# Kernel optimization log

Hardware: AMD Instinct MI355X
Metric: run time of the kernel (lower is better)

Reference implementation:

```python
import jax, jax.numpy as jnp
import numpy as np

N_NODES = 100000


def _gcn_conv(x, W, b, src, dst, num_nodes):
    """PyG GCNConv: h = x @ W; symmetric-normalized scatter-add over edges
    (self-loops already included in src/dst); out = aggregate + b."""
    h = x @ W  # [N, out]
    ones = jnp.ones(src.shape[0], dtype=x.dtype)
    deg = jax.ops.segment_sum(ones, dst, num_segments=num_nodes)  # in-degree incl self-loop
    dinv = jnp.where(deg > 0, jax.lax.rsqrt(deg), 0.0)
    norm = dinv[src] * dinv[dst]  # [E]
    msg = h[src] * norm[:, None]  # [E, out] -- dominant memory traffic
    out = jax.ops.segment_sum(msg, dst, num_segments=num_nodes)
    return out + b


def setup_inputs() -> dict:
    key = jax.random.key(0)
    k = jax.random.split(key, 4)
    in_c, hid, out_c = 128, 64, 32
    n_edges = 1600000
    x = jax.random.normal(k[0], (N_NODES, in_c), dtype=jnp.float32)
    edge_index = jax.random.randint(k[1], (2, n_edges), 0, N_NODES, dtype=jnp.int64)
    W1 = jax.random.normal(k[2], (in_c, hid), dtype=jnp.float32) * (1.0 / np.sqrt(in_c))
    b1 = jnp.zeros((hid,), dtype=jnp.float32)
    W2 = jax.random.normal(k[3], (hid, out_c), dtype=jnp.float32) * (1.0 / np.sqrt(hid))
    b2 = jnp.zeros((out_c,), dtype=jnp.float32)
    return {"x": x, "edge_index": edge_index, "W1": W1, "b1": b1, "W2": W2, "b2": b2}


def reference(x, edge_index, W1, b1, W2, b2):
    num_nodes = x.shape[0]
    loops = jnp.arange(num_nodes, dtype=edge_index.dtype)
    src = jnp.concatenate([edge_index[0], loops])  # add self-loops once, shared by both layers
    dst = jnp.concatenate([edge_index[1], loops])
    h = _gcn_conv(x, W1, b1, src, dst, num_nodes)
    h = jax.nn.relu(h)
    out = _gcn_conv(h, W2, b2, src, dst, num_nodes)
    return out
```

## Files before the change

### kernel.cpp

```cpp
#include <hip/hip_runtime.h>


#define NBKT(n) (((n) + 127) >> 7)

__device__ inline float bf2f(unsigned short u) {
    union { unsigned int i; float f; } v;
    v.i = ((unsigned int)u) << 16;
    return v.f;
}
__device__ inline unsigned short f2bf(float f) {
    union { float f; unsigned int i; } v;
    v.f = f;
    unsigned int u = v.i;
    return (unsigned short)((u + 0x7fff + ((u >> 16) & 1)) >> 16);
}

#define BH_CHUNK 4096
__global__ void __launch_bounds__(256) bhist_kernel(
        const int* __restrict__ dst, int E, int nbk, int* __restrict__ bcnt) {
    __shared__ int cnt[NBKT(100000)];
    const int t = threadIdx.x;
    const int beg = blockIdx.x * BH_CHUNK;
    const int end = min(E, beg + BH_CHUNK);
    for (int b = t; b < nbk; b += 256) cnt[b] = 0;
    __syncthreads();
    for (int i = beg + t; i < end; i += 256) atomicAdd(&cnt[dst[i] >> 7], 1);
    __syncthreads();
    for (int b = t; b < nbk; b += 256) {
        int c = cnt[b];
        if (c) atomicAdd(&bcnt[b], c);
    }
}

__global__ void bscan_kernel(const int* __restrict__ bcnt, int nbk, int E,
                             int* __restrict__ boffs, int* __restrict__ gcursor) {
    __shared__ int s[1024];
    const int t = threadIdx.x;
    int v = (t < nbk) ? bcnt[t] : 0;
    s[t] = v;
    __syncthreads();
    for (int off = 1; off < 1024; off <<= 1) {
        int x = (t >= off) ? s[t - off] : 0;
        __syncthreads();
        s[t] += x;
        __syncthreads();
    }
    if (t < nbk) {
        int excl = s[t] - v;
        boffs[t] = excl;
        gcursor[t] = excl;
    }
    if (t == 0) boffs[nbk] = E;
}

#define BF_CHUNK 4096
__global__ void __launch_bounds__(256) binfill_kernel(
        const int* __restrict__ src, const int* __restrict__ dst, int E, int nbk,
        int* __restrict__ gcursor, int* __restrict__ entries) {
    __shared__ int cnt[NBKT(100000)];
    __shared__ int gbase[NBKT(100000)];
    __shared__ int rank[NBKT(100000)];
    const int t = threadIdx.x;
    const int beg = blockIdx.x * BF_CHUNK;
    const int end = min(E, beg + BF_CHUNK);
    for (int b = t; b < nbk; b += 256) cnt[b] = 0;
    __syncthreads();
    for (int i = beg + t; i < end; i += 256) atomicAdd(&cnt[dst[i] >> 7], 1);
    __syncthreads();
    for (int b = t; b < nbk; b += 256) {
        int c = cnt[b];
        gbase[b] = c ? atomicAdd(&gcursor[b], c) : 0;
        rank[b] = 0;
    }
    __syncthreads();
    for (int i = beg + t; i < end; i += 256) {
        int d = dst[i];
        int b = d >> 7;
        int r = atomicAdd(&rank[b], 1);
        entries[gbase[b] + r] = (src[i] << 7) | (d & 127);
    }
}

__global__ void __launch_bounds__(256) bucket2csr_kernel(
        const int* __restrict__ entries, const int* __restrict__ boffs, int nbk,
        int* __restrict__ offs, int* __restrict__ csr_src, float* __restrict__ dinv,
        int N, int E) {
    __shared__ int cnt[128];
    __shared__ int s[128];
    __shared__ int rank[128];
    const int t = threadIdx.x;
    const int b = blockIdx.x;
    const int beg = boffs[b];
    const int end = boffs[b + 1];
    if (t < 128) { cnt[t] = 0; rank[t] = 0; }
    __syncthreads();
    for (int i = beg + t; i < end; i += 256) atomicAdd(&cnt[entries[i] & 127], 1);
    __syncthreads();
    if (t < 128) s[t] = cnt[t];
    __syncthreads();
    for (int off = 1; off < 128; off <<= 1) {
        int x = 0;
        if (t < 128 && t >= off) x = s[t - off];
        __syncthreads();
        if (t < 128) s[t] += x;
        __syncthreads();
    }
    const int node0 = b * 128;
    if (t < 128 && node0 + t < N) {
        offs[node0 + t] = beg + s[t] - cnt[t];
        dinv[node0 + t] = rsqrtf((float)cnt[t] + 1.0f);
    }
    if (b == 0 && t == 0) offs[N] = E;
    __syncthreads();
    for (int i = beg + t; i < end; i += 256) {
        int e = entries[i];
        int d = e & 127;
        int r = atomicAdd(&rank[d], 1);
        csr_src[beg + s[d] - cnt[d] + r] = (int)((unsigned)e >> 7);
    }
}

#define FMA4(ACC, AV, WV) \
    ACC.x += (AV) * (WV).x; ACC.y += (AV) * (WV).y; ACC.z += (AV) * (WV).z; ACC.w += (AV) * (WV).w;

template <int K, int C, int BR, bool BF16OUT, bool BF16IN>
__global__ void __launch_bounds__(256) gemm_tile_kernel(
        const void* __restrict__ Av, const float* __restrict__ W,
        const float* __restrict__ dinv, void* __restrict__ outv, int N) {
    constexpr int F4R = K / 4;
    constexpr int CG = C / 4;
    static_assert(256 / CG * 4 == BR, "geometry");
    __shared__ float Wl[K * C];
    __shared__ float Al[BR * K];

    const int t = threadIdx.x;
    for (int i = t; i < K * C / 4; i += 256) ((float4*)Wl)[i] = ((const float4*)W)[i];
    const int row0 = blockIdx.x * BR;
    for (int i = t; i < BR * F4R; i += 256) {
        int r = i / F4R, k4 = i % F4R;
        float4 v = make_float4(0.f, 0.f, 0.f, 0.f);
        if (row0 + r < N) {
            if (BF16IN) {
                ushort4 u = ((const ushort4*)Av)[(size_t)(row0 + r) * F4R + k4];
                v.x = bf2f(u.x); v.y = bf2f(u.y); v.z = bf2f(u.z); v.w = bf2f(u.w);
            } else {
                v = ((const float4*)Av)[(size_t)(row0 + r) * F4R + k4];
            }
        }
        *(float4*)(Al + r * K + k4 * 4) = v;
    }
    __syncthreads();

    const int c0 = (t % CG) * 4;
    const int r0 = (t / CG) * 4;
    const float* Ab = Al + r0 * K;

    float4 acc0 = {0, 0, 0, 0}, acc1 = {0, 0, 0, 0}, acc2 = {0, 0, 0, 0}, acc3 = {0, 0, 0, 0};

#pragma unroll 2
    for (int k4 = 0; k4 < K / 4; ++k4) {
        float4 a0 = *(const float4*)(Ab + 0 * K + k4 * 4);
        float4 a1 = *(const float4*)(Ab + 1 * K + k4 * 4);
        float4 a2 = *(const float4*)(Ab + 2 * K + k4 * 4);
        float4 a3 = *(const float4*)(Ab + 3 * K + k4 * 4);
        float4 w0 = *(const float4*)(Wl + (k4 * 4 + 0) * C + c0);
        float4 w1 = *(const float4*)(Wl + (k4 * 4 + 1) * C + c0);
        float4 w2 = *(const float4*)(Wl + (k4 * 4 + 2) * C + c0);
        float4 w3 = *(const float4*)(Wl + (k4 * 4 + 3) * C + c0);
        FMA4(acc0, a0.x, w0) FMA4(acc1, a1.x, w0) FMA4(acc2, a2.x, w0) FMA4(acc3, a3.x, w0)
        FMA4(acc0, a0.y, w1) FMA4(acc1, a1.y, w1) FMA4(acc2, a2.y, w1) FMA4(acc3, a3.y, w1)
        FMA4(acc0, a0.z, w2) FMA4(acc1, a1.z, w2) FMA4(acc2, a2.z, w2) FMA4(acc3, a3.z, w2)
        FMA4(acc0, a0.w, w3) FMA4(acc1, a1.w, w3) FMA4(acc2, a2.w, w3) FMA4(acc3, a3.w, w3)
    }

    const int row = row0 + r0;
#pragma unroll
    for (int i = 0; i < 4; ++i) {
        int rr = row + i;
        if (rr < N) {
            float d = dinv[rr];
            float4 fr = (i == 0) ? acc0 : (i == 1) ? acc1 : (i == 2) ? acc2 : acc3;
            fr.x *= d; fr.y *= d; fr.z *= d; fr.w *= d;
            if (BF16OUT) {
                ushort4 o;
                o.x = f2bf(fr.x); o.y = f2bf(fr.y); o.z = f2bf(fr.z); o.w = f2bf(fr.w);
                *(ushort4*)((unsigned short*)outv + (size_t)rr * C + c0) = o;
            } else {
                *(float4*)((float*)outv + (size_t)rr * C + c0) = fr;
            }
        }
    }
}

#define G64_LOAD(SS) bf2f(hs[(size_t)(SS) * 64 + lane])
__global__ void __launch_bounds__(256) gather64_kernel(
        const unsigned short* __restrict__ hs, const float* __restrict__ dinv,
        const int* __restrict__ offs, const int* __restrict__ csr_src,
        const float* __restrict__ b, unsigned short* __restrict__ out, int N) {
    const int lane = threadIdx.x & 63;
    const int d = blockIdx.x * 4 + (threadIdx.x >> 6);
    if (d >= N) return;
    const int beg = offs[d];
    const int end = offs[d + 1];
    float acc0 = G64_LOAD(d);
    float acc1 = 0.f, acc2 = 0.f, acc3 = 0.f;
    int j = beg;
    for (; j + 15 < end; j += 16) {
        int s0 = csr_src[j + 0], s1 = csr_src[j + 1], s2 = csr_src[j + 2], s3 = csr_src[j + 3];
        int s4 = csr_src[j + 4], s5 = csr_src[j + 5], s6 = csr_src[j + 6], s7 = csr_src[j + 7];
        int s8 = csr_src[j + 8], s9 = csr_src[j + 9], sa = csr_src[j + 10], sb = csr_src[j + 11];
        int sc = csr_src[j + 12], sd = csr_src[j + 13], se = csr_src[j + 14], sf = csr_src[j + 15];
        float v0 = G64_LOAD(s0), v1 = G64_LOAD(s1), v2 = G64_LOAD(s2), v3 = G64_LOAD(s3);
        float v4 = G64_LOAD(s4), v5 = G64_LOAD(s5), v6 = G64_LOAD(s6), v7 = G64_LOAD(s7);
        float v8 = G64_LOAD(s8), v9 = G64_LOAD(s9), va = G64_LOAD(sa), vb = G64_LOAD(sb);
        float vc = G64_LOAD(sc), vd = G64_LOAD(sd), ve = G64_LOAD(se), vf = G64_LOAD(sf);
        acc0 += v0; acc1 += v1; acc2 += v2; acc3 += v3;
        acc0 += v4; acc1 += v5; acc2 += v6; acc3 += v7;
        acc0 += v8; acc1 += v9; acc2 += va; acc3 += vb;
        acc0 += vc; acc1 += vd; acc2 += ve; acc3 += vf;
    }
    if (j + 7 < end) {
        int s0 = csr_src[j + 0], s1 = csr_src[j + 1], s2 = csr_src[j + 2], s3 = csr_src[j + 3];
        int s4 = csr_src[j + 4], s5 = csr_src[j + 5], s6 = csr_src[j + 6], s7 = csr_src[j + 7];
        float v0 = G64_LOAD(s0), v1 = G64_LOAD(s1), v2 = G64_LOAD(s2), v3 = G64_LOAD(s3);
        float v4 = G64_LOAD(s4), v5 = G64_LOAD(s5), v6 = G64_LOAD(s6), v7 = G64_LOAD(s7);
        acc0 += v0; acc1 += v1; acc2 += v2; acc3 += v3;
        acc0 += v4; acc1 += v5; acc2 += v6; acc3 += v7;
        j += 8;
    }
    if (j + 3 < end) {
        int s0 = csr_src[j + 0], s1 = csr_src[j + 1], s2 = csr_src[j + 2], s3 = csr_src[j + 3];
        acc0 += G64_LOAD(s0); acc1 += G64_LOAD(s1); acc2 += G64_LOAD(s2); acc3 += G64_LOAD(s3);
        j += 4;
    }
    for (; j < end; ++j) acc0 += G64_LOAD(csr_src[j]);
    float r = ((acc0 + acc1) + (acc2 + acc3)) * dinv[d] + b[lane];
    r = fmaxf(r, 0.f);
    out[(size_t)d * 64 + lane] = f2bf(r);
}

#define G32_LOAD(SS) bf2f(hs[(size_t)(SS) * 32 + lane])
__global__ void __launch_bounds__(256) gather32_kernel(
        const unsigned short* __restrict__ hs, const float* __restrict__ dinv,
        const int* __restrict__ offs, const int* __restrict__ csr_src,
        const float* __restrict__ b, float* __restrict__ out, int N) {
    const int lane = threadIdx.x & 31;
    const int d = blockIdx.x * 8 + (threadIdx.x >> 5);
    if (d >= N) return;
    const int beg = offs[d];
    const int end = offs[d + 1];
    float acc0 = G32_LOAD(d);
    float acc1 = 0.f, acc2 = 0.f, acc3 = 0.f;
    int j = beg;
    for (; j + 15 < end; j += 16) {
        int s0 = csr_src[j + 0], s1 = csr_src[j + 1], s2 = csr_src[j + 2], s3 = csr_src[j + 3];
        int s4 = csr_src[j + 4], s5 = csr_src[j + 5], s6 = csr_src[j + 6], s7 = csr_src[j + 7];
        int s8 = csr_src[j + 8], s9 = csr_src[j + 9], sa = csr_src[j + 10], sb = csr_src[j + 11];
        int sc = csr_src[j + 12], sd = csr_src[j + 13], se = csr_src[j + 14], sf = csr_src[j + 15];
        float v0 = G32_LOAD(s0), v1 = G32_LOAD(s1), v2 = G32_LOAD(s2), v3 = G32_LOAD(s3);
        float v4 = G32_LOAD(s4), v5 = G32_LOAD(s5), v6 = G32_LOAD(s6), v7 = G32_LOAD(s7);
        float v8 = G32_LOAD(s8), v9 = G32_LOAD(s9), va = G32_LOAD(sa), vb = G32_LOAD(sb);
        float vc = G32_LOAD(sc), vd = G32_LOAD(sd), ve = G32_LOAD(se), vf = G32_LOAD(sf);
        acc0 += v0; acc1 += v1; acc2 += v2; acc3 += v3;
        acc0 += v4; acc1 += v5; acc2 += v6; acc3 += v7;
        acc0 += v8; acc1 += v9; acc2 += va; acc3 += vb;
        acc0 += vc; acc1 += vd; acc2 += ve; acc3 += vf;
    }
    if (j + 7 < end) {
        int s0 = csr_src[j + 0], s1 = csr_src[j + 1], s2 = csr_src[j + 2], s3 = csr_src[j + 3];
        int s4 = csr_src[j + 4], s5 = csr_src[j + 5], s6 = csr_src[j + 6], s7 = csr_src[j + 7];
        float v0 = G32_LOAD(s0), v1 = G32_LOAD(s1), v2 = G32_LOAD(s2), v3 = G32_LOAD(s3);
        float v4 = G32_LOAD(s4), v5 = G32_LOAD(s5), v6 = G32_LOAD(s6), v7 = G32_LOAD(s7);
        acc0 += v0; acc1 += v1; acc2 += v2; acc3 += v3;
        acc0 += v4; acc1 += v5; acc2 += v6; acc3 += v7;
        j += 8;
    }
    if (j + 3 < end) {
        int s0 = csr_src[j + 0], s1 = csr_src[j + 1], s2 = csr_src[j + 2], s3 = csr_src[j + 3];
        acc0 += G32_LOAD(s0); acc1 += G32_LOAD(s1); acc2 += G32_LOAD(s2); acc3 += G32_LOAD(s3);
        j += 4;
    }
    for (; j < end; ++j) acc0 += G32_LOAD(csr_src[j]);
    float r = ((acc0 + acc1) + (acc2 + acc3)) * dinv[d] + b[lane];
    out[(size_t)d * 32 + lane] = r;
}

extern "C" void kernel_launch(void* const* d_in, const int* in_sizes, int n_in,
                              void* d_out, int out_size, void* d_ws, size_t ws_size,
                              hipStream_t stream) {
    const float* x = (const float*)d_in[0];
    const int* ei = (const int*)d_in[1];
    const float* W1 = (const float*)d_in[2];
    const float* b1 = (const float*)d_in[3];
    const float* W2 = (const float*)d_in[4];
    const float* b2 = (const float*)d_in[5];

    const int N = in_sizes[0] / 128;
    const int E = in_sizes[1] / 2;
    const int* src = ei;
    const int* dst = ei + E;
    const int nbk = NBKT(N);

    int* bcnt = (int*)d_ws;
    int* boffs = bcnt + 1024;
    int* gcursor = boffs + 1024;
    float* dinv = (float*)(gcursor + 1024);
    int* offs = (int*)(dinv + ((N + 255) & ~255));
    int* entries = offs + ((N + 1 + 255) & ~255);
    int* csr_src = entries + ((E + 255) & ~255);
    unsigned short* h1s = (unsigned short*)(csr_src + ((E + 255) & ~255));
    unsigned short* h2b = h1s + (size_t)N * 64;
    unsigned short* h3s = h1s;
    float* out = (float*)d_out;

    hipMemsetAsync(bcnt, 0, 1024 * 4, stream);
    bhist_kernel<<<(E + BH_CHUNK - 1) / BH_CHUNK, 256, 0, stream>>>(dst, E, nbk, bcnt);
    bscan_kernel<<<1, 1024, 0, stream>>>(bcnt, nbk, E, boffs, gcursor);

    binfill_kernel<<<(E + BF_CHUNK - 1) / BF_CHUNK, 256, 0, stream>>>(src, dst, E, nbk, gcursor, entries);
    bucket2csr_kernel<<<nbk, 256, 0, stream>>>(entries, boffs, nbk, offs, csr_src, dinv, N, E);

    gemm_tile_kernel<128, 64, 64, true, false><<<(N + 63) / 64, 256, 0, stream>>>(x, W1, dinv, h1s, N);

    gather64_kernel<<<(N + 3) / 4, 256, 0, stream>>>(h1s, dinv, offs, csr_src, b1, h2b, N);

    gemm_tile_kernel<64, 32, 128, true, true><<<(N + 127) / 128, 256, 0, stream>>>(h2b, W2, dinv, h3s, N);

    gather32_kernel<<<(N + 7) / 8, 256, 0, stream>>>(h3s, dinv, offs, csr_src, b2, out, N);
}
```

Before: 203.0 us.

## Overlap first GEMM with CSR build by co-launching in fused kernels

The first dense GEMM (x@W1) no longer needs dinv, so it is split in half and its blocks are appended to the binfill and bucket2csr launches, running concurrently with graph preprocessing. To make this possible, the source-side dinv scaling moves into the layer-1 gather, which now loads dinv[src] per edge. The aim is to fill idle CUs during the latency-bound CSR build and to save a launch. The cost is extra per-edge dinv gathers in gather64 and a larger 64KB static shared allocation for the binning blocks, which may lower their occupancy.

```diff
diff --git a/kernel.cpp b/kernel.cpp
--- a/kernel.cpp
+++ b/kernel.cpp
@@ -53,100 +53,20 @@
     if (t == 0) boffs[nbk] = E;
 }
 
-#define BF_CHUNK 4096
-__global__ void __launch_bounds__(256) binfill_kernel(
-        const int* __restrict__ src, const int* __restrict__ dst, int E, int nbk,
-        int* __restrict__ gcursor, int* __restrict__ entries) {
-    __shared__ int cnt[NBKT(100000)];
-    __shared__ int gbase[NBKT(100000)];
-    __shared__ int rank[NBKT(100000)];
-    const int t = threadIdx.x;
-    const int beg = blockIdx.x * BF_CHUNK;
-    const int end = min(E, beg + BF_CHUNK);
-    for (int b = t; b < nbk; b += 256) cnt[b] = 0;
-    __syncthreads();
-    for (int i = beg + t; i < end; i += 256) atomicAdd(&cnt[dst[i] >> 7], 1);
-    __syncthreads();
-    for (int b = t; b < nbk; b += 256) {
-        int c = cnt[b];
-        gbase[b] = c ? atomicAdd(&gcursor[b], c) : 0;
-        rank[b] = 0;
-    }
-    __syncthreads();
-    for (int i = beg + t; i < end; i += 256) {
-        int d = dst[i];
-        int b = d >> 7;
-        int r = atomicAdd(&rank[b], 1);
-        entries[gbase[b] + r] = (src[i] << 7) | (d & 127);
-    }
-}
-
-__global__ void __launch_bounds__(256) bucket2csr_kernel(
-        const int* __restrict__ entries, const int* __restrict__ boffs, int nbk,
-        int* __restrict__ offs, int* __restrict__ csr_src, float* __restrict__ dinv,
-        int N, int E) {
-    __shared__ int cnt[128];
-    __shared__ int s[128];
-    __shared__ int rank[128];
-    const int t = threadIdx.x;
-    const int b = blockIdx.x;
-    const int beg = boffs[b];
-    const int end = boffs[b + 1];
-    if (t < 128) { cnt[t] = 0; rank[t] = 0; }
-    __syncthreads();
-    for (int i = beg + t; i < end; i += 256) atomicAdd(&cnt[entries[i] & 127], 1);
-    __syncthreads();
-    if (t < 128) s[t] = cnt[t];
-    __syncthreads();
-    for (int off = 1; off < 128; off <<= 1) {
-        int x = 0;
-        if (t < 128 && t >= off) x = s[t - off];
-        __syncthreads();
-        if (t < 128) s[t] += x;
-        __syncthreads();
-    }
-    const int node0 = b * 128;
-    if (t < 128 && node0 + t < N) {
-        offs[node0 + t] = beg + s[t] - cnt[t];
-        dinv[node0 + t] = rsqrtf((float)cnt[t] + 1.0f);
-    }
-    if (b == 0 && t == 0) offs[N] = E;
-    __syncthreads();
-    for (int i = beg + t; i < end; i += 256) {
-        int e = entries[i];
-        int d = e & 127;
-        int r = atomicAdd(&rank[d], 1);
-        csr_src[beg + s[d] - cnt[d] + r] = (int)((unsigned)e >> 7);
-    }
-}
-
 #define FMA4(ACC, AV, WV) \
     ACC.x += (AV) * (WV).x; ACC.y += (AV) * (WV).y; ACC.z += (AV) * (WV).z; ACC.w += (AV) * (WV).w;
 
-template <int K, int C, int BR, bool BF16OUT, bool BF16IN>
-__global__ void __launch_bounds__(256) gemm_tile_kernel(
-        const void* __restrict__ Av, const float* __restrict__ W,
-        const float* __restrict__ dinv, void* __restrict__ outv, int N) {
-    constexpr int F4R = K / 4;
-    constexpr int CG = C / 4;
-    static_assert(256 / CG * 4 == BR, "geometry");
-    __shared__ float Wl[K * C];
-    __shared__ float Al[BR * K];
-
+__device__ __forceinline__ void gemm1_body(
+        const float* __restrict__ A, const float* __restrict__ W,
+        unsigned short* __restrict__ out, int N, int row0,
+        float* Wl, float* Al) {
+    constexpr int K = 128, C = 64, F4R = 32, CG = 16;
     const int t = threadIdx.x;
     for (int i = t; i < K * C / 4; i += 256) ((float4*)Wl)[i] = ((const float4*)W)[i];
-    const int row0 = blockIdx.x * BR;
-    for (int i = t; i < BR * F4R; i += 256) {
+    for (int i = t; i < 64 * F4R; i += 256) {
         int r = i / F4R, k4 = i % F4R;
         float4 v = make_float4(0.f, 0.f, 0.f, 0.f);
-        if (row0 + r < N) {
-            if (BF16IN) {
-                ushort4 u = ((const ushort4*)Av)[(size_t)(row0 + r) * F4R + k4];
-                v.x = bf2f(u.x); v.y = bf2f(u.y); v.z = bf2f(u.z); v.w = bf2f(u.w);
-            } else {
-                v = ((const float4*)Av)[(size_t)(row0 + r) * F4R + k4];
-            }
-        }
+        if (row0 + r < N) v = ((const float4*)A)[(size_t)(row0 + r) * F4R + k4];
         *(float4*)(Al + r * K + k4 * 4) = v;
     }
     __syncthreads();
@@ -154,7 +74,6 @@
     const int c0 = (t % CG) * 4;
     const int r0 = (t / CG) * 4;
     const float* Ab = Al + r0 * K;
-
     float4 acc0 = {0, 0, 0, 0}, acc1 = {0, 0, 0, 0}, acc2 = {0, 0, 0, 0}, acc3 = {0, 0, 0, 0};
 
 #pragma unroll 2
@@ -178,16 +97,153 @@
     for (int i = 0; i < 4; ++i) {
         int rr = row + i;
         if (rr < N) {
+            float4 fr = (i == 0) ? acc0 : (i == 1) ? acc1 : (i == 2) ? acc2 : acc3;
+            ushort4 o;
+            o.x = f2bf(fr.x); o.y = f2bf(fr.y); o.z = f2bf(fr.z); o.w = f2bf(fr.w);
+            *(ushort4*)(out + (size_t)rr * C + c0) = o;
+        }
+    }
+}
+
+#define BF_CHUNK 4096
+__global__ void __launch_bounds__(256) fusedA_kernel(
+        const int* __restrict__ src, const int* __restrict__ dst, int E, int nbk,
+        int* __restrict__ gcursor, int* __restrict__ entries, int nBin,
+        const float* __restrict__ x, const float* __restrict__ W1,
+        unsigned short* __restrict__ h1u, int N) {
+    __shared__ float smem[16384];
+    if ((int)blockIdx.x < nBin) {
+        int* cnt = (int*)smem;
+        int* gbase = cnt + NBKT(100000);
+        int* rank = gbase + NBKT(100000);
+        const int t = threadIdx.x;
+        const int beg = blockIdx.x * BF_CHUNK;
+        const int end = min(E, beg + BF_CHUNK);
+        for (int b = t; b < nbk; b += 256) cnt[b] = 0;
+        __syncthreads();
+        for (int i = beg + t; i < end; i += 256) atomicAdd(&cnt[dst[i] >> 7], 1);
+        __syncthreads();
+        for (int b = t; b < nbk; b += 256) {
+            int c = cnt[b];
+            gbase[b] = c ? atomicAdd(&gcursor[b], c) : 0;
+            rank[b] = 0;
+        }
+        __syncthreads();
+        for (int i = beg + t; i < end; i += 256) {
+            int d = dst[i];
+            int b = d >> 7;
+            int r = atomicAdd(&rank[b], 1);
+            entries[gbase[b] + r] = (src[i] << 7) | (d & 127);
+        }
+    } else {
+        int row0 = (blockIdx.x - nBin) * 64;
+        gemm1_body(x, W1, h1u, N, row0, smem, smem + 128 * 64);
+    }
+}
+
+__global__ void __launch_bounds__(256) fusedB_kernel(
+        const int* __restrict__ entries, const int* __restrict__ boffs, int nbk,
+        int* __restrict__ offs, int* __restrict__ csr_src, float* __restrict__ dinv,
+        int N, int E,
+        const float* __restrict__ x, const float* __restrict__ W1,
+        unsigned short* __restrict__ h1u, int rowBase) {
+    __shared__ float smem[16384];
+    if ((int)blockIdx.x < nbk) {
+        int* cnt = (int*)smem;
+        int* s = cnt + 128;
+        int* rank = s + 128;
+        const int t = threadIdx.x;
+        const int b = blockIdx.x;
+        const int beg = boffs[b];
+        const int end = boffs[b + 1];
+        if (t < 128) { cnt[t] = 0; rank[t] = 0; }
+        __syncthreads();
+        for (int i = beg + t; i < end; i += 256) atomicAdd(&cnt[entries[i] & 127], 1);
+        __syncthreads();
+        if (t < 128) s[t] = cnt[t];
+        __syncthreads();
+        for (int off = 1; off < 128; off <<= 1) {
+            int x2 = 0;
+            if (t < 128 && t >= off) x2 = s[t - off];
+            __syncthreads();
+            if (t < 128) s[t] += x2;
+            __syncthreads();
+        }
+        const int node0 = b * 128;
+        if (t < 128 && node0 + t < N) {
+            offs[node0 + t] = beg + s[t] - cnt[t];
+            dinv[node0 + t] = rsqrtf((float)cnt[t] + 1.0f);
+        }
+        if (b == 0 && t == 0) offs[N] = E;
+        __syncthreads();
+        for (int i = beg + t; i < end; i += 256) {
+            int e = entries[i];
+            int d = e & 127;
+            int r = atomicAdd(&rank[d], 1);
+            csr_src[beg + s[d] - cnt[d] + r] = (int)((unsigned)e >> 7);
+        }
+    } else {
+        int row0 = rowBase + (blockIdx.x - nbk) * 64;
+        gemm1_body(x, W1, h1u, N, row0, smem, smem + 128 * 64);
+    }
+}
+
+template <int K, int C, int BR>
+__global__ void __launch_bounds__(256) gemm2_kernel(
+        const unsigned short* __restrict__ A, const float* __restrict__ W,
+        const float* __restrict__ dinv, unsigned short* __restrict__ out, int N) {
+    constexpr int F4R = K / 4;
+    constexpr int CG = C / 4;
+    static_assert(256 / CG * 4 == BR, "geometry");
+    __shared__ float Wl[K * C];
+    __shared__ float Al[BR * K];
+
+    const int t = threadIdx.x;
+    for (int i = t; i < K * C / 4; i += 256) ((float4*)Wl)[i] = ((const float4*)W)[i];
+    const int row0 = blockIdx.x * BR;
+    for (int i = t; i < BR * F4R; i += 256) {
+        int r = i / F4R, k4 = i % F4R;
+        float4 v = make_float4(0.f, 0.f, 0.f, 0.f);
+        if (row0 + r < N) {
+            ushort4 u = ((const ushort4*)A)[(size_t)(row0 + r) * F4R + k4];
+            v.x = bf2f(u.x); v.y = bf2f(u.y); v.z = bf2f(u.z); v.w = bf2f(u.w);
+        }
+        *(float4*)(Al + r * K + k4 * 4) = v;
+    }
+    __syncthreads();
+
+    const int c0 = (t % CG) * 4;
+    const int r0 = (t / CG) * 4;
+    const float* Ab = Al + r0 * K;
+    float4 acc0 = {0, 0, 0, 0}, acc1 = {0, 0, 0, 0}, acc2 = {0, 0, 0, 0}, acc3 = {0, 0, 0, 0};
+
+#pragma unroll 2
+    for (int k4 = 0; k4 < K / 4; ++k4) {
+        float4 a0 = *(const float4*)(Ab + 0 * K + k4 * 4);
+        float4 a1 = *(const float4*)(Ab + 1 * K + k4 * 4);
+        float4 a2 = *(const float4*)(Ab + 2 * K + k4 * 4);
+        float4 a3 = *(const float4*)(Ab + 3 * K + k4 * 4);
+        float4 w0 = *(const float4*)(Wl + (k4 * 4 + 0) * C + c0);
+        float4 w1 = *(const float4*)(Wl + (k4 * 4 + 1) * C + c0);
+        float4 w2 = *(const float4*)(Wl + (k4 * 4 + 2) * C + c0);
+        float4 w3 = *(const float4*)(Wl + (k4 * 4 + 3) * C + c0);
+        FMA4(acc0, a0.x, w0) FMA4(acc1, a1.x, w0) FMA4(acc2, a2.x, w0) FMA4(acc3, a3.x, w0)
+        FMA4(acc0, a0.y, w1) FMA4(acc1, a1.y, w1) FMA4(acc2, a2.y, w1) FMA4(acc3, a3.y, w1)
+        FMA4(acc0, a0.z, w2) FMA4(acc1, a1.z, w2) FMA4(acc2, a2.z, w2) FMA4(acc3, a3.z, w2)
+        FMA4(acc0, a0.w, w3) FMA4(acc1, a1.w, w3) FMA4(acc2, a2.w, w3) FMA4(acc3, a3.w, w3)
+    }
+
+    const int row = row0 + r0;
+#pragma unroll
+    for (int i = 0; i < 4; ++i) {
+        int rr = row + i;
+        if (rr < N) {
             float d = dinv[rr];
             float4 fr = (i == 0) ? acc0 : (i == 1) ? acc1 : (i == 2) ? acc2 : acc3;
-            fr.x *= d; fr.y *= d; fr.z *= d; fr.w *= d;
-            if (BF16OUT) {
-                ushort4 o;
-                o.x = f2bf(fr.x); o.y = f2bf(fr.y); o.z = f2bf(fr.z); o.w = f2bf(fr.w);
-                *(ushort4*)((unsigned short*)outv + (size_t)rr * C + c0) = o;
-            } else {
-                *(float4*)((float*)outv + (size_t)rr * C + c0) = fr;
-            }
+            ushort4 o;
+            o.x = f2bf(fr.x * d); o.y = f2bf(fr.y * d);
+            o.z = f2bf(fr.z * d); o.w = f2bf(fr.w * d);
+            *(ushort4*)(out + (size_t)rr * C + c0) = o;
         }
     }
 }
@@ -202,7 +258,8 @@
     if (d >= N) return;
     const int beg = offs[d];
     const int end = offs[d + 1];
-    float acc0 = G64_LOAD(d);
+    const float dv = dinv[d];
+    float acc0 = G64_LOAD(d) * dv;
     float acc1 = 0.f, acc2 = 0.f, acc3 = 0.f;
     int j = beg;
     for (; j + 15 < end; j += 16) {
@@ -210,31 +267,42 @@
         int s4 = csr_src[j + 4], s5 = csr_src[j + 5], s6 = csr_src[j + 6], s7 = csr_src[j + 7];
         int s8 = csr_src[j + 8], s9 = csr_src[j + 9], sa = csr_src[j + 10], sb = csr_src[j + 11];
         int sc = csr_src[j + 12], sd = csr_src[j + 13], se = csr_src[j + 14], sf = csr_src[j + 15];
+        float w0 = dinv[s0], w1 = dinv[s1], w2 = dinv[s2], w3 = dinv[s3];
+        float w4 = dinv[s4], w5 = dinv[s5], w6 = dinv[s6], w7 = dinv[s7];
+        float w8 = dinv[s8], w9 = dinv[s9], wa = dinv[sa], wb = dinv[sb];
+        float wc = dinv[sc], wd = dinv[sd], we = dinv[se], wf = dinv[sf];
         float v0 = G64_LOAD(s0), v1 = G64_LOAD(s1), v2 = G64_LOAD(s2), v3 = G64_LOAD(s3);
         float v4 = G64_LOAD(s4), v5 = G64_LOAD(s5), v6 = G64_LOAD(s6), v7 = G64_LOAD(s7);
         float v8 = G64_LOAD(s8), v9 = G64_LOAD(s9), va = G64_LOAD(sa), vb = G64_LOAD(sb);
         float vc = G64_LOAD(sc), vd = G64_LOAD(sd), ve = G64_LOAD(se), vf = G64_LOAD(sf);
-        acc0 += v0; acc1 += v1; acc2 += v2; acc3 += v3;
-        acc0 += v4; acc1 += v5; acc2 += v6; acc3 += v7;
-        acc0 += v8; acc1 += v9; acc2 += va; acc3 += vb;
-        acc0 += vc; acc1 += vd; acc2 += ve; acc3 += vf;
+        acc0 += v0 * w0; acc1 += v1 * w1; acc2 += v2 * w2; acc3 += v3 * w3;
+        acc0 += v4 * w4; acc1 += v5 * w5; acc2 += v6 * w6; acc3 += v7 * w7;
+        acc0 += v8 * w8; acc1 += v9 * w9; acc2 += va * wa; acc3 += vb * wb;
+        acc0 += vc * wc; acc1 += vd * wd; acc2 += ve * we; acc3 += vf * wf;
     }
     if (j + 7 < end) {
         int s0 = csr_src[j + 0], s1 = csr_src[j + 1], s2 = csr_src[j + 2], s3 = csr_src[j + 3];
         int s4 = csr_src[j + 4], s5 = csr_src[j + 5], s6 = csr_src[j + 6], s7 = csr_src[j + 7];
+        float w0 = dinv[s0], w1 = dinv[s1], w2 = dinv[s2], w3 = dinv[s3];
+        float w4 = dinv[s4], w5 = dinv[s5], w6 = dinv[s6], w7 = dinv[s7];
         float v0 = G64_LOAD(s0), v1 = G64_LOAD(s1), v2 = G64_LOAD(s2), v3 = G64_LOAD(s3);
         float v4 = G64_LOAD(s4), v5 = G64_LOAD(s5), v6 = G64_LOAD(s6), v7 = G64_LOAD(s7);
-        acc0 += v0; acc1 += v1; acc2 += v2; acc3 += v3;
-        acc0 += v4; acc1 += v5; acc2 += v6; acc3 += v7;
+        acc0 += v0 * w0; acc1 += v1 * w1; acc2 += v2 * w2; acc3 += v3 * w3;
+        acc0 += v4 * w4; acc1 += v5 * w5; acc2 += v6 * w6; acc3 += v7 * w7;
         j += 8;
     }
     if (j + 3 < end) {
         int s0 = csr_src[j + 0], s1 = csr_src[j + 1], s2 = csr_src[j + 2], s3 = csr_src[j + 3];
-        acc0 += G64_LOAD(s0); acc1 += G64_LOAD(s1); acc2 += G64_LOAD(s2); acc3 += G64_LOAD(s3);
+        float w0 = dinv[s0], w1 = dinv[s1], w2 = dinv[s2], w3 = dinv[s3];
+        acc0 += G64_LOAD(s0) * w0; acc1 += G64_LOAD(s1) * w1;
+        acc2 += G64_LOAD(s2) * w2; acc3 += G64_LOAD(s3) * w3;
         j += 4;
     }
-    for (; j < end; ++j) acc0 += G64_LOAD(csr_src[j]);
-    float r = ((acc0 + acc1) + (acc2 + acc3)) * dinv[d] + b[lane];
+    for (; j < end; ++j) {
+        int s = csr_src[j];
+        acc0 += G64_LOAD(s) * dinv[s];
+    }
+    float r = ((acc0 + acc1) + (acc2 + acc3)) * dv + b[lane];
     r = fmaxf(r, 0.f);
     out[(size_t)d * 64 + lane] = f2bf(r);
 }
@@ -308,23 +376,30 @@
     int* offs = (int*)(dinv + ((N + 255) & ~255));
     int* entries = offs + ((N + 1 + 255) & ~255);
     int* csr_src = entries + ((E + 255) & ~255);
-    unsigned short* h1s = (unsigned short*)(csr_src + ((E + 255) & ~255));
-    unsigned short* h2b = h1s + (size_t)N * 64;
-    unsigned short* h3s = h1s;
+    unsigned short* h1u = (unsigned short*)(csr_src + ((E + 255) & ~255));
+    unsigned short* h2b = h1u + (size_t)N * 64;
+    unsigned short* h3s = h1u;
     float* out = (float*)d_out;
+
+    const int nBin = (E + BF_CHUNK - 1) / BF_CHUNK;
+    const int GB = (N + 63) / 64;
+    const int GA = GB / 2;
+    const int GBB = GB - GA;
+    const int rowBase = GA * 64;
 
     hipMemsetAsync(bcnt, 0, 1024 * 4, stream);
     bhist_kernel<<<(E + BH_CHUNK - 1) / BH_CHUNK, 256, 0, stream>>>(dst, E, nbk, bcnt);
     bscan_kernel<<<1, 1024, 0, stream>>>(bcnt, nbk, E, boffs, gcursor);
 
-    binfill_kernel<<<(E + BF_CHUNK - 1) / BF_CHUNK, 256, 0, stream>>>(src, dst, E, nbk, gcursor, entries);
-    bucket2csr_kernel<<<nbk, 256, 0, stream>>>(entries, boffs, nbk, offs, csr_src, dinv, N, E);
-
-    gemm_tile_kernel<128, 64, 64, true, false><<<(N + 63) / 64, 256, 0, stream>>>(x, W1, dinv, h1s, N);
-
-    gather64_kernel<<<(N + 3) / 4, 256, 0, stream>>>(h1s, dinv, offs, csr_src, b1, h2b, N);
-
-    gemm_tile_kernel<64, 32, 128, true, true><<<(N + 127) / 128, 256, 0, stream>>>(h2b, W2, dinv, h3s, N);
+    fusedA_kernel<<<nBin + GA, 256, 0, stream>>>(src, dst, E, nbk, gcursor, entries, nBin,
+                                                 x, W1, h1u, N);
+
+    fusedB_kernel<<<nbk + GBB, 256, 0, stream>>>(entries, boffs, nbk, offs, csr_src, dinv,
+                                                 N, E, x, W1, h1u, rowBase);
+
+    gather64_kernel<<<(N + 3) / 4, 256, 0, stream>>>(h1u, dinv, offs, csr_src, b1, h2b, N);
+
+    gemm2_kernel<64, 32, 128><<<(N + 127) / 128, 256, 0, stream>>>(h2b, W2, dinv, h3s, N);
 
     gather32_kernel<<<(N + 7) / 8, 256, 0, stream>>>(h3s, dinv, offs, csr_src, b2, out, N);
 }
```

Result: slower. 211.4 us (+4.1%).
